# Kernel tuning notes

Hardware: AMD Instinct MI355X
Metric: run time of the kernel (lower is better)

## Reference

```python
import jax, jax.numpy as jnp
import numpy as np

OUTLINER_RATIO = 0.01
SUB_OUTLINER_BIT = 8
NEG_INF = -1e9


def setup_inputs() -> dict:
    key = jax.random.key(0)
    T, H, D = 4096, 8, 64
    qkv = jax.random.normal(key, (T, 3, H, D), dtype=jnp.float32)
    cu_seqlens = jnp.array([0, 1024, 2048, 3072, 4096], dtype=jnp.int32)
    return {"qkv": qkv, "cu_seqlens": cu_seqlens, "max_seqlen": 1024}


def _varlen_attention(q, k, v, cu_seqlens, causal=False):
    # q,k,v: [T, H, D]; sequences delimited by cu_seqlens (attention never
    # crosses segment boundaries, matching flash_attn_varlen semantics).
    T, H, D = q.shape
    scale = D ** (-0.5)
    pos = jnp.arange(T)
    seg = jnp.searchsorted(cu_seqlens, pos, side="right") - 1  # [T] segment ids
    mask = seg[:, None] == seg[None, :]                          # [T, T]
    if causal:
        mask = mask & (pos[:, None] >= pos[None, :])
    scores = jnp.einsum("thd,shd->hts", q, k) * scale            # [H, T, T]
    scores = jnp.where(mask[None, :, :], scores, NEG_INF)
    probs = jax.nn.softmax(scores, axis=-1)
    out = jnp.einsum("hts,shd->thd", probs, v)                   # [T, H, D]
    return out


def _outlier_quant_compress(x, outliner_ratio=OUTLINER_RATIO, bit=SUB_OUTLINER_BIT):
    # Outlier detection: keep top-ratio |x| entries in full precision;
    # quantize the residual (sub-outliers) to `bit` bits per-tensor.
    a = jnp.abs(x)
    thr = jnp.quantile(a.reshape(-1), 1.0 - outliner_ratio)
    outliers = jnp.where(a > thr, x, 0.0)
    resid = x - outliers
    qmax = 2.0 ** (bit - 1) - 1.0
    scale = jnp.maximum(jnp.max(jnp.abs(resid)), 1e-8) / qmax
    q = jnp.clip(jnp.round(resid / scale), -qmax, qmax)
    x_hat = outliers + q * scale  # decompressed approximation
    return x_hat, thr, scale


def reference(qkv, cu_seqlens, max_seqlen):
    q, k, v = qkv[:, 0], qkv[:, 1], qkv[:, 2]
    out = _varlen_attention(q, k, v, cu_seqlens, causal=False)
    # Compression pipeline (stats + quantize) runs on Q,K,V,O in the original
    # forward; it does not alter the forward output.
    for t in (q, k, v, out):
        _outlier_quant_compress(t)
    return out
```

## Files before the change

kernel.cpp:

```cpp
#include <hip/hip_runtime.h>


#define HEADS 8
#define DH 64
#define TQ 64
#define TK 64
#define PSTR 72
#define NEG_BIG -1e30f
#define L2E 1.44269504088896340736f

using f32x4 = __attribute__((ext_vector_type(4))) float;
using s16x8 = __attribute__((ext_vector_type(8))) short;

__device__ inline unsigned short bf16b(float x) {
    union { float f; unsigned u; } c; c.f = x;
    unsigned r = c.u + 0x7fffu + ((c.u >> 16) & 1u);
    return (unsigned short)(r >> 16);
}

#if __has_builtin(__builtin_amdgcn_cvt_pk_bf16_f32)
__device__ inline unsigned pk2(float a, float b) {
    auto v = __builtin_amdgcn_cvt_pk_bf16_f32(a, b);
    unsigned u; __builtin_memcpy(&u, &v, 4); return u;
}
#else
__device__ inline unsigned pk2(float a, float b) {
    return (unsigned)bf16b(a) | ((unsigned)bf16b(b) << 16);
}
#endif

__global__ __launch_bounds__(256)
void prep_kernel(const float* __restrict__ qkv, unsigned short* __restrict__ Qb,
                 unsigned short* __restrict__ Kb, unsigned short* __restrict__ Vtb,
                 int T) {
    __shared__ unsigned short Lt[64][PSTR];
    const int m = blockIdx.z, h = blockIdx.y, t0 = blockIdx.x * 64;
    const int tid = threadIdx.x, d8 = tid & 7, tr = tid >> 3;

    #pragma unroll
    for (int i = 0; i < 2; ++i) {
        int t = t0 + i * 32 + tr;
        int tc = t < T ? t : T - 1;
        const float* src = qkv + ((size_t)tc * 3 + m) * (HEADS * DH) + h * DH + d8 * 8;
        float4 a = *(const float4*)src;
        float4 b = *(const float4*)(src + 4);
        if (m == 0) {
            a.x *= 0.125f; a.y *= 0.125f; a.z *= 0.125f; a.w *= 0.125f;
            b.x *= 0.125f; b.y *= 0.125f; b.z *= 0.125f; b.w *= 0.125f;
        }
        unsigned p0 = pk2(a.x, a.y), p1 = pk2(a.z, a.w);
        unsigned p2 = pk2(b.x, b.y), p3 = pk2(b.z, b.w);
        if (m == 2) {
            *(uint2*)&Lt[i * 32 + tr][d8 * 8]     = make_uint2(p0, p1);
            *(uint2*)&Lt[i * 32 + tr][d8 * 8 + 4] = make_uint2(p2, p3);
        } else if (t < T) {
            unsigned short* dst = (m == 0)
                ? (Qb + (size_t)t * (HEADS * DH) + h * DH + d8 * 8)
                : (Kb + ((size_t)h * T + t) * DH + d8 * 8);
            *(uint4*)dst = make_uint4(p0, p1, p2, p3);
        }
    }
    if (m == 2) {
        __syncthreads();
        const int d = tid >> 2, tg = tid & 3;
        #pragma unroll
        for (int p = 0; p < 2; ++p) {
            int G = tg + 4 * p;
            int td = t0 + G * 8;
            unsigned u[4];
            #pragma unroll
            for (int jj = 0; jj < 4; ++jj)
                u[jj] = (unsigned)Lt[G * 8 + 2 * jj][d] |
                        ((unsigned)Lt[G * 8 + 2 * jj + 1][d] << 16);
            if (td < T)
                *(uint4*)(Vtb + ((size_t)h * DH + d) * T + td) =
                    make_uint4(u[0], u[1], u[2], u[3]);
        }
    }
}

__global__ __launch_bounds__(256, 4)
void fa_main(const unsigned short* __restrict__ Qb, const unsigned short* __restrict__ Kb,
             const unsigned short* __restrict__ Vtb, const int* __restrict__ cu,
             int n_cu, int T, float* __restrict__ out,
             float* __restrict__ Opart, float* __restrict__ Mp, float* __restrict__ Lp) {
    __shared__ unsigned short Ksh[TK * DH];
    __shared__ unsigned short Vsh[DH * TK];
    __shared__ unsigned short Psh[TQ][PSTR];

    const int tid = threadIdx.x;
    const int h = blockIdx.y, t0 = blockIdx.x * TQ;
    const int split = blockIdx.z, nsplit = gridDim.z;
    const int w = tid >> 6, lane = tid & 63, n15 = lane & 15, quad = lane >> 4;

    int trow = t0 + w * 16 + n15; if (trow > T - 1) trow = T - 1;
    int lo, hi;
    { int s = 0; for (int j = 1; j < n_cu - 1; ++j) if (cu[j] <= trow) s = j;
      lo = cu[s]; hi = cu[s + 1]; }
    int kb_, ke;
    { int s = 0; for (int j = 1; j < n_cu - 1; ++j) if (cu[j] <= t0) s = j;
      kb_ = cu[s];
      int tl = t0 + TQ - 1; if (tl > T - 1) tl = T - 1;
      s = 0; for (int j = 1; j < n_cu - 1; ++j) if (cu[j] <= tl) s = j;
      ke = cu[s + 1]; }

    s16x8 qfrag[2];
    {
        int tc = t0 + w * 16 + n15; if (tc > T - 1) tc = T - 1;
        const unsigned short* qp = Qb + (size_t)tc * (HEADS * DH) + h * DH + quad * 8;
        qfrag[0] = *(const s16x8*)qp;
        qfrag[1] = *(const s16x8*)(qp + 32);
    }

    const unsigned short* kb_h = Kb + (size_t)h * T * DH;
    const unsigned short* vt_h = Vtb + (size_t)h * DH * T;
    int krow_rel[2], vkey_off[2];
    const unsigned short* kbase[2];
    const unsigned short* vbase[2];
    #pragma unroll
    for (int i = 0; i < 2; ++i) {
        int gg = i * 64 + lane;
        int rr = gg >> 3;
        int gc = gg & 7;
        int row = w * 16 + rr;
        int gcol = gc ^ (row & 7);
        krow_rel[i] = row;
        kbase[i] = kb_h + gcol * 8;
        vbase[i] = vt_h + (size_t)row * T;
        vkey_off[i] = gcol * 8;
    }
    int off16[2];
    #pragma unroll
    for (int kh = 0; kh < 2; ++kh)
        off16[kh] = n15 * 128 + (((kh * 4 + quad) ^ (n15 & 7)) * 16);

    f32x4 oacc[4];
    #pragma unroll
    for (int i = 0; i < 4; ++i) oacc[i] = (f32x4){0.f, 0.f, 0.f, 0.f};
    float m_ = NEG_BIG, l_ = 0.f;

    const int c0_start = (kb_ / TK) * TK + split * TK;
    for (int c0 = c0_start; c0 < ke; c0 += nsplit * TK) {
        #pragma unroll
        for (int i = 0; i < 2; ++i) {
            int rk = c0 + krow_rel[i]; if (rk > T - 1) rk = T - 1;
            __builtin_amdgcn_global_load_lds(
                (const __attribute__((address_space(1))) void*)(kbase[i] + ((size_t)rk << 6)),
                (__attribute__((address_space(3))) void*)&Ksh[(w * 128 + i * 64) * 8],
                16, 0, 0);
            int kv = c0 + vkey_off[i]; if (kv > T - 8) kv = T - 8;
            __builtin_amdgcn_global_load_lds(
                (const __attribute__((address_space(1))) void*)(vbase[i] + kv),
                (__attribute__((address_space(3))) void*)&Vsh[(w * 128 + i * 64) * 8],
                16, 0, 0);
        }
        __syncthreads();

        const char* Kc = (const char*)Ksh;
        f32x4 sacc[4];
        #pragma unroll
        for (int nt = 0; nt < 4; ++nt) {
            s16x8 k0 = *(const s16x8*)(Kc + nt * 2048 + off16[0]);
            s16x8 k1 = *(const s16x8*)(Kc + nt * 2048 + off16[1]);
            f32x4 z = (f32x4){0.f, 0.f, 0.f, 0.f};
            z = __builtin_amdgcn_mfma_f32_16x16x32_bf16(k0, qfrag[0], z, 0, 0, 0);
            z = __builtin_amdgcn_mfma_f32_16x16x32_bf16(k1, qfrag[1], z, 0, 0, 0);
            sacc[nt] = z;
        }

        if (!(c0 >= lo && c0 + TK <= hi)) {
            #pragma unroll
            for (int nt = 0; nt < 4; ++nt)
                #pragma unroll
                for (int reg = 0; reg < 4; ++reg) {
                    int key = c0 + nt * 16 + quad * 4 + reg;
                    bool valid = (key >= lo) && (key < hi);
                    sacc[nt][reg] = valid ? sacc[nt][reg] : NEG_BIG;
                }
        }

        float rm = NEG_BIG;
        #pragma unroll
        for (int nt = 0; nt < 4; ++nt)
            #pragma unroll
            for (int reg = 0; reg < 4; ++reg) rm = fmaxf(rm, sacc[nt][reg]);
        rm = fmaxf(rm, __shfl_xor(rm, 16));
        rm = fmaxf(rm, __shfl_xor(rm, 32));
        float mn = fmaxf(m_, rm);
        float alpha = exp2f((m_ - mn) * L2E);
        float mnl = mn * L2E;
        float rs = 0.f;
        #pragma unroll
        for (int nt = 0; nt < 4; ++nt) {
            float p0 = exp2f(fmaf(sacc[nt][0], L2E, -mnl));
            float p1 = exp2f(fmaf(sacc[nt][1], L2E, -mnl));
            float p2 = exp2f(fmaf(sacc[nt][2], L2E, -mnl));
            float p3 = exp2f(fmaf(sacc[nt][3], L2E, -mnl));
            rs += (p0 + p1) + (p2 + p3);
            *(uint2*)&Psh[w * 16 + n15][nt * 16 + quad * 4] =
                make_uint2(pk2(p0, p1), pk2(p2, p3));
        }
        rs += __shfl_xor(rs, 16);
        rs += __shfl_xor(rs, 32);
        l_ = fmaf(l_, alpha, rs);
        m_ = mn;
        #pragma unroll
        for (int reg = 0; reg < 4; ++reg) {
            float ar = __shfl(alpha, quad * 4 + reg);
            oacc[0][reg] *= ar; oacc[1][reg] *= ar;
            oacc[2][reg] *= ar; oacc[3][reg] *= ar;
        }

        s16x8 afr[2];
        afr[0] = *(const s16x8*)&Psh[w * 16 + n15][quad * 8];
        afr[1] = *(const s16x8*)&Psh[w * 16 + n15][32 + quad * 8];
        const char* Vc = (const char*)Vsh;
        #pragma unroll
        for (int nt = 0; nt < 4; ++nt) {
            s16x8 v0 = *(const s16x8*)(Vc + nt * 2048 + off16[0]);
            s16x8 v1 = *(const s16x8*)(Vc + nt * 2048 + off16[1]);
            oacc[nt] = __builtin_amdgcn_mfma_f32_16x16x32_bf16(afr[0], v0, oacc[nt], 0, 0, 0);
            oacc[nt] = __builtin_amdgcn_mfma_f32_16x16x32_bf16(afr[1], v1, oacc[nt], 0, 0, 0);
        }
        __syncthreads();
    }

    if (nsplit == 1) {
        #pragma unroll
        for (int reg = 0; reg < 4; ++reg) {
            float lr = __shfl(l_, quad * 4 + reg);
            float inv = 1.f / fmaxf(lr, 1e-30f);
            int t = t0 + w * 16 + quad * 4 + reg;
            if (t < T) {
                #pragma unroll
                for (int nt = 0; nt < 4; ++nt)
                    out[((size_t)t * HEADS + h) * DH + nt * 16 + n15] = oacc[nt][reg] * inv;
            }
        }
    } else {
        #pragma unroll
        for (int reg = 0; reg < 4; ++reg) {
            int t = t0 + w * 16 + quad * 4 + reg;
            if (t < T) {
                size_t base = (((size_t)split * T + t) * HEADS + h) * DH;
                #pragma unroll
                for (int nt = 0; nt < 4; ++nt)
                    Opart[base + nt * 16 + n15] = oacc[nt][reg];
            }
        }
        int tq = t0 + w * 16 + n15;
        if (quad == 0 && tq < T) {
            size_t mi = ((size_t)split * T + tq) * HEADS + h;
            Mp[mi] = m_; Lp[mi] = l_;
        }
    }
}

__global__ __launch_bounds__(256)
void fa_combine_kernel(const float* __restrict__ Opart, const float* __restrict__ Mp,
                       const float* __restrict__ Lp, float* __restrict__ out, int T) {
    int i4 = blockIdx.x * blockDim.x + threadIdx.x;
    int total = T * HEADS * (DH / 4);
    if (i4 >= total) return;
    int th = i4 / (DH / 4);
    int d4 = i4 - th * (DH / 4);
    size_t stride = (size_t)T * HEADS * DH;
    int mlstride = T * HEADS;
    float m0 = Mp[th], m1 = Mp[mlstride + th];
    float l0 = Lp[th], l1 = Lp[mlstride + th];
    float M = fmaxf(m0, m1);
    float w0 = exp2f((m0 - M) * L2E);
    float w1 = exp2f((m1 - M) * L2E);
    float L = fmaxf(fmaf(l0, w0, l1 * w1), 1e-30f);
    float inv = 1.f / L;
    size_t off = (size_t)th * DH + 4 * d4;
    float4 a = *(const float4*)&Opart[off];
    float4 b = *(const float4*)&Opart[stride + off];
    float4 o;
    o.x = fmaf(a.x, w0, b.x * w1) * inv;
    o.y = fmaf(a.y, w0, b.y * w1) * inv;
    o.z = fmaf(a.z, w0, b.z * w1) * inv;
    o.w = fmaf(a.w, w0, b.w * w1) * inv;
    *(float4*)&out[off] = o;
}

extern "C" void kernel_launch(void* const* d_in, const int* in_sizes, int n_in,
                              void* d_out, int out_size, void* d_ws, size_t ws_size,
                              hipStream_t stream) {
    const float* qkv = (const float*)d_in[0];
    const int* cu    = (const int*)d_in[1];
    const int n_cu   = in_sizes[1];
    const int T      = in_sizes[0] / (3 * HEADS * DH);
    float* out       = (float*)d_out;

    const int NSPLIT = 2;
    size_t elems = (size_t)T * HEADS * DH;

    float* Opart = (float*)d_ws;
    float* Mpp   = Opart + (size_t)NSPLIT * elems;
    float* Lpp   = Mpp + (size_t)NSPLIT * T * HEADS;
    unsigned short* Qb  = (unsigned short*)(Lpp + (size_t)NSPLIT * T * HEADS);
    unsigned short* Kb  = Qb + elems;
    unsigned short* Vtb = Kb + elems;

    int tiles = (T + TQ - 1) / TQ;
    dim3 pgrid(tiles, HEADS, 3);
    prep_kernel<<<pgrid, 256, 0, stream>>>(qkv, Qb, Kb, Vtb, T);

    dim3 grid(tiles, HEADS, NSPLIT);
    fa_main<<<grid, 256, 0, stream>>>(Qb, Kb, Vtb, cu, n_cu, T, out, Opart, Mpp, Lpp);

    int total4 = T * HEADS * (DH / 4);
    fa_combine_kernel<<<(total4 + 255) / 256, 256, 0, stream>>>(Opart, Mpp, Lpp, out, T);
}
```

Before: 105.9 us.

## Double query tile per block to reuse K/V loads and raise KV split count to four

Each warp now processes two 16-row query subtiles (TQ 128), so every K/V tile staged in shared memory feeds twice as many MFMAs. To keep enough blocks in flight, the KV dimension is split four ways instead of two, and the combine kernel is generalized to merge NSPLIT partial results. This trades more registers per thread and larger partial-output traffic (4x Opart) for less K/V load work per query; the prep kernel keeps its 64-row tiling.

```diff
diff --git a/kernel.cpp b/kernel.cpp
--- a/kernel.cpp
+++ b/kernel.cpp
@@ -3,9 +3,10 @@
 
 #define HEADS 8
 #define DH 64
-#define TQ 64
+#define TQ 128
 #define TK 64
 #define PSTR 72
+#define NSPLIT 4
 #define NEG_BIG -1e30f
 #define L2E 1.44269504088896340736f
 
@@ -93,10 +94,14 @@
     const int split = blockIdx.z, nsplit = gridDim.z;
     const int w = tid >> 6, lane = tid & 63, n15 = lane & 15, quad = lane >> 4;
 
-    int trow = t0 + w * 16 + n15; if (trow > T - 1) trow = T - 1;
-    int lo, hi;
-    { int s = 0; for (int j = 1; j < n_cu - 1; ++j) if (cu[j] <= trow) s = j;
-      lo = cu[s]; hi = cu[s + 1]; }
+    int lo[2], hi[2];
+    #pragma unroll
+    for (int mt = 0; mt < 2; ++mt) {
+        int trow = t0 + w * 32 + mt * 16 + n15; if (trow > T - 1) trow = T - 1;
+        int s = 0;
+        for (int j = 1; j < n_cu - 1; ++j) if (cu[j] <= trow) s = j;
+        lo[mt] = cu[s]; hi[mt] = cu[s + 1];
+    }
     int kb_, ke;
     { int s = 0; for (int j = 1; j < n_cu - 1; ++j) if (cu[j] <= t0) s = j;
       kb_ = cu[s];
@@ -104,12 +109,13 @@
       s = 0; for (int j = 1; j < n_cu - 1; ++j) if (cu[j] <= tl) s = j;
       ke = cu[s + 1]; }
 
-    s16x8 qfrag[2];
-    {
-        int tc = t0 + w * 16 + n15; if (tc > T - 1) tc = T - 1;
+    s16x8 qfrag[2][2];
+    #pragma unroll
+    for (int mt = 0; mt < 2; ++mt) {
+        int tc = t0 + w * 32 + mt * 16 + n15; if (tc > T - 1) tc = T - 1;
         const unsigned short* qp = Qb + (size_t)tc * (HEADS * DH) + h * DH + quad * 8;
-        qfrag[0] = *(const s16x8*)qp;
-        qfrag[1] = *(const s16x8*)(qp + 32);
+        qfrag[mt][0] = *(const s16x8*)qp;
+        qfrag[mt][1] = *(const s16x8*)(qp + 32);
     }
 
     const unsigned short* kb_h = Kb + (size_t)h * T * DH;
@@ -134,10 +140,12 @@
     for (int kh = 0; kh < 2; ++kh)
         off16[kh] = n15 * 128 + (((kh * 4 + quad) ^ (n15 & 7)) * 16);
 
-    f32x4 oacc[4];
-    #pragma unroll
-    for (int i = 0; i < 4; ++i) oacc[i] = (f32x4){0.f, 0.f, 0.f, 0.f};
-    float m_ = NEG_BIG, l_ = 0.f;
+    f32x4 oacc[2][4];
+    #pragma unroll
+    for (int mt = 0; mt < 2; ++mt)
+        #pragma unroll
+        for (int i = 0; i < 4; ++i) oacc[mt][i] = (f32x4){0.f, 0.f, 0.f, 0.f};
+    float m_[2] = {NEG_BIG, NEG_BIG}, l_[2] = {0.f, 0.f};
 
     const int c0_start = (kb_ / TK) * TK + split * TK;
     for (int c0 = c0_start; c0 < ke; c0 += nsplit * TK) {
@@ -157,101 +165,116 @@
         __syncthreads();
 
         const char* Kc = (const char*)Ksh;
-        f32x4 sacc[4];
+        f32x4 sacc[2][4];
         #pragma unroll
         for (int nt = 0; nt < 4; ++nt) {
             s16x8 k0 = *(const s16x8*)(Kc + nt * 2048 + off16[0]);
             s16x8 k1 = *(const s16x8*)(Kc + nt * 2048 + off16[1]);
-            f32x4 z = (f32x4){0.f, 0.f, 0.f, 0.f};
-            z = __builtin_amdgcn_mfma_f32_16x16x32_bf16(k0, qfrag[0], z, 0, 0, 0);
-            z = __builtin_amdgcn_mfma_f32_16x16x32_bf16(k1, qfrag[1], z, 0, 0, 0);
-            sacc[nt] = z;
-        }
-
-        if (!(c0 >= lo && c0 + TK <= hi)) {
+            #pragma unroll
+            for (int mt = 0; mt < 2; ++mt) {
+                f32x4 z = (f32x4){0.f, 0.f, 0.f, 0.f};
+                z = __builtin_amdgcn_mfma_f32_16x16x32_bf16(k0, qfrag[mt][0], z, 0, 0, 0);
+                z = __builtin_amdgcn_mfma_f32_16x16x32_bf16(k1, qfrag[mt][1], z, 0, 0, 0);
+                sacc[mt][nt] = z;
+            }
+        }
+
+        #pragma unroll
+        for (int mt = 0; mt < 2; ++mt) {
+            if (!(c0 >= lo[mt] && c0 + TK <= hi[mt])) {
+                #pragma unroll
+                for (int nt = 0; nt < 4; ++nt)
+                    #pragma unroll
+                    for (int reg = 0; reg < 4; ++reg) {
+                        int key = c0 + nt * 16 + quad * 4 + reg;
+                        bool valid = (key >= lo[mt]) && (key < hi[mt]);
+                        sacc[mt][nt][reg] = valid ? sacc[mt][nt][reg] : NEG_BIG;
+                    }
+            }
+            float rm = NEG_BIG;
             #pragma unroll
             for (int nt = 0; nt < 4; ++nt)
                 #pragma unroll
-                for (int reg = 0; reg < 4; ++reg) {
-                    int key = c0 + nt * 16 + quad * 4 + reg;
-                    bool valid = (key >= lo) && (key < hi);
-                    sacc[nt][reg] = valid ? sacc[nt][reg] : NEG_BIG;
-                }
-        }
-
-        float rm = NEG_BIG;
-        #pragma unroll
-        for (int nt = 0; nt < 4; ++nt)
-            #pragma unroll
-            for (int reg = 0; reg < 4; ++reg) rm = fmaxf(rm, sacc[nt][reg]);
-        rm = fmaxf(rm, __shfl_xor(rm, 16));
-        rm = fmaxf(rm, __shfl_xor(rm, 32));
-        float mn = fmaxf(m_, rm);
-        float alpha = exp2f((m_ - mn) * L2E);
-        float mnl = mn * L2E;
-        float rs = 0.f;
-        #pragma unroll
-        for (int nt = 0; nt < 4; ++nt) {
-            float p0 = exp2f(fmaf(sacc[nt][0], L2E, -mnl));
-            float p1 = exp2f(fmaf(sacc[nt][1], L2E, -mnl));
-            float p2 = exp2f(fmaf(sacc[nt][2], L2E, -mnl));
-            float p3 = exp2f(fmaf(sacc[nt][3], L2E, -mnl));
-            rs += (p0 + p1) + (p2 + p3);
-            *(uint2*)&Psh[w * 16 + n15][nt * 16 + quad * 4] =
-                make_uint2(pk2(p0, p1), pk2(p2, p3));
-        }
-        rs += __shfl_xor(rs, 16);
-        rs += __shfl_xor(rs, 32);
-        l_ = fmaf(l_, alpha, rs);
-        m_ = mn;
-        #pragma unroll
-        for (int reg = 0; reg < 4; ++reg) {
-            float ar = __shfl(alpha, quad * 4 + reg);
-            oacc[0][reg] *= ar; oacc[1][reg] *= ar;
-            oacc[2][reg] *= ar; oacc[3][reg] *= ar;
-        }
-
-        s16x8 afr[2];
-        afr[0] = *(const s16x8*)&Psh[w * 16 + n15][quad * 8];
-        afr[1] = *(const s16x8*)&Psh[w * 16 + n15][32 + quad * 8];
+                for (int reg = 0; reg < 4; ++reg) rm = fmaxf(rm, sacc[mt][nt][reg]);
+            rm = fmaxf(rm, __shfl_xor(rm, 16));
+            rm = fmaxf(rm, __shfl_xor(rm, 32));
+            float mn = fmaxf(m_[mt], rm);
+            float alpha = exp2f((m_[mt] - mn) * L2E);
+            float mnl = mn * L2E;
+            float rs = 0.f;
+            int prow = w * 32 + mt * 16 + n15;
+            #pragma unroll
+            for (int nt = 0; nt < 4; ++nt) {
+                float p0 = exp2f(fmaf(sacc[mt][nt][0], L2E, -mnl));
+                float p1 = exp2f(fmaf(sacc[mt][nt][1], L2E, -mnl));
+                float p2 = exp2f(fmaf(sacc[mt][nt][2], L2E, -mnl));
+                float p3 = exp2f(fmaf(sacc[mt][nt][3], L2E, -mnl));
+                rs += (p0 + p1) + (p2 + p3);
+                *(uint2*)&Psh[prow][nt * 16 + quad * 4] =
+                    make_uint2(pk2(p0, p1), pk2(p2, p3));
+            }
+            rs += __shfl_xor(rs, 16);
+            rs += __shfl_xor(rs, 32);
+            l_[mt] = fmaf(l_[mt], alpha, rs);
+            m_[mt] = mn;
+            #pragma unroll
+            for (int reg = 0; reg < 4; ++reg) {
+                float ar = __shfl(alpha, quad * 4 + reg);
+                oacc[mt][0][reg] *= ar; oacc[mt][1][reg] *= ar;
+                oacc[mt][2][reg] *= ar; oacc[mt][3][reg] *= ar;
+            }
+        }
+
+        s16x8 afr[2][2];
+        #pragma unroll
+        for (int mt = 0; mt < 2; ++mt) {
+            afr[mt][0] = *(const s16x8*)&Psh[w * 32 + mt * 16 + n15][quad * 8];
+            afr[mt][1] = *(const s16x8*)&Psh[w * 32 + mt * 16 + n15][32 + quad * 8];
+        }
         const char* Vc = (const char*)Vsh;
         #pragma unroll
         for (int nt = 0; nt < 4; ++nt) {
             s16x8 v0 = *(const s16x8*)(Vc + nt * 2048 + off16[0]);
             s16x8 v1 = *(const s16x8*)(Vc + nt * 2048 + off16[1]);
-            oacc[nt] = __builtin_amdgcn_mfma_f32_16x16x32_bf16(afr[0], v0, oacc[nt], 0, 0, 0);
-            oacc[nt] = __builtin_amdgcn_mfma_f32_16x16x32_bf16(afr[1], v1, oacc[nt], 0, 0, 0);
+            #pragma unroll
+            for (int mt = 0; mt < 2; ++mt) {
+                oacc[mt][nt] = __builtin_amdgcn_mfma_f32_16x16x32_bf16(afr[mt][0], v0, oacc[mt][nt], 0, 0, 0);
+                oacc[mt][nt] = __builtin_amdgcn_mfma_f32_16x16x32_bf16(afr[mt][1], v1, oacc[mt][nt], 0, 0, 0);
+            }
         }
         __syncthreads();
     }
 
-    if (nsplit == 1) {
-        #pragma unroll
-        for (int reg = 0; reg < 4; ++reg) {
-            float lr = __shfl(l_, quad * 4 + reg);
-            float inv = 1.f / fmaxf(lr, 1e-30f);
-            int t = t0 + w * 16 + quad * 4 + reg;
-            if (t < T) {
-                #pragma unroll
-                for (int nt = 0; nt < 4; ++nt)
-                    out[((size_t)t * HEADS + h) * DH + nt * 16 + n15] = oacc[nt][reg] * inv;
-            }
-        }
-    } else {
-        #pragma unroll
-        for (int reg = 0; reg < 4; ++reg) {
-            int t = t0 + w * 16 + quad * 4 + reg;
-            if (t < T) {
-                size_t base = (((size_t)split * T + t) * HEADS + h) * DH;
-                #pragma unroll
-                for (int nt = 0; nt < 4; ++nt)
-                    Opart[base + nt * 16 + n15] = oacc[nt][reg];
-            }
-        }
-        int tq = t0 + w * 16 + n15;
-        if (quad == 0 && tq < T) {
-            size_t mi = ((size_t)split * T + tq) * HEADS + h;
-            Mp[mi] = m_; Lp[mi] = l_;
+    #pragma unroll
+    for (int mt = 0; mt < 2; ++mt) {
+        if (nsplit == 1) {
+            #pragma unroll
+            for (int reg = 0; reg < 4; ++reg) {
+                float lr = __shfl(l_[mt], quad * 4 + reg);
+                float inv = 1.f / fmaxf(lr, 1e-30f);
+                int t = t0 + w * 32 + mt * 16 + quad * 4 + reg;
+                if (t < T) {
+                    #pragma unroll
+                    for (int nt = 0; nt < 4; ++nt)
+                        out[((size_t)t * HEADS + h) * DH + nt * 16 + n15] = oacc[mt][nt][reg] * inv;
+                }
+            }
+        } else {
+            #pragma unroll
+            for (int reg = 0; reg < 4; ++reg) {
+                int t = t0 + w * 32 + mt * 16 + quad * 4 + reg;
+                if (t < T) {
+                    size_t base = (((size_t)split * T + t) * HEADS + h) * DH;
+                    #pragma unroll
+                    for (int nt = 0; nt < 4; ++nt)
+                        Opart[base + nt * 16 + n15] = oacc[mt][nt][reg];
+                }
+            }
+            int tq = t0 + w * 32 + mt * 16 + n15;
+            if (quad == 0 && tq < T) {
+                size_t mi = ((size_t)split * T + tq) * HEADS + h;
+                Mp[mi] = m_[mt]; Lp[mi] = l_[mt];
+            }
         }
     }
 }
@@ -266,21 +289,31 @@
     int d4 = i4 - th * (DH / 4);
     size_t stride = (size_t)T * HEADS * DH;
     int mlstride = T * HEADS;
-    float m0 = Mp[th], m1 = Mp[mlstride + th];
-    float l0 = Lp[th], l1 = Lp[mlstride + th];
-    float M = fmaxf(m0, m1);
-    float w0 = exp2f((m0 - M) * L2E);
-    float w1 = exp2f((m1 - M) * L2E);
-    float L = fmaxf(fmaf(l0, w0, l1 * w1), 1e-30f);
-    float inv = 1.f / L;
+    float m[NSPLIT], l[NSPLIT];
+    float M = NEG_BIG;
+    #pragma unroll
+    for (int s = 0; s < NSPLIT; ++s) {
+        m[s] = Mp[(size_t)s * mlstride + th];
+        l[s] = Lp[(size_t)s * mlstride + th];
+        M = fmaxf(M, m[s]);
+    }
+    float L = 0.f, wgt[NSPLIT];
+    #pragma unroll
+    for (int s = 0; s < NSPLIT; ++s) {
+        wgt[s] = exp2f((m[s] - M) * L2E);
+        L = fmaf(l[s], wgt[s], L);
+    }
+    float inv = 1.f / fmaxf(L, 1e-30f);
     size_t off = (size_t)th * DH + 4 * d4;
-    float4 a = *(const float4*)&Opart[off];
-    float4 b = *(const float4*)&Opart[stride + off];
-    float4 o;
-    o.x = fmaf(a.x, w0, b.x * w1) * inv;
-    o.y = fmaf(a.y, w0, b.y * w1) * inv;
-    o.z = fmaf(a.z, w0, b.z * w1) * inv;
-    o.w = fmaf(a.w, w0, b.w * w1) * inv;
+    float4 o = make_float4(0.f, 0.f, 0.f, 0.f);
+    #pragma unroll
+    for (int s = 0; s < NSPLIT; ++s) {
+        float4 a = *(const float4*)&Opart[(size_t)s * stride + off];
+        float ws = wgt[s];
+        o.x = fmaf(a.x, ws, o.x); o.y = fmaf(a.y, ws, o.y);
+        o.z = fmaf(a.z, ws, o.z); o.w = fmaf(a.w, ws, o.w);
+    }
+    o.x *= inv; o.y *= inv; o.z *= inv; o.w *= inv;
     *(float4*)&out[off] = o;
 }
 
@@ -293,7 +326,6 @@
     const int T      = in_sizes[0] / (3 * HEADS * DH);
     float* out       = (float*)d_out;
 
-    const int NSPLIT = 2;
     size_t elems = (size_t)T * HEADS * DH;
 
     float* Opart = (float*)d_ws;
@@ -303,10 +335,11 @@
     unsigned short* Kb  = Qb + elems;
     unsigned short* Vtb = Kb + elems;
 
+    int ptiles = (T + 63) / 64;
+    dim3 pgrid(ptiles, HEADS, 3);
+    prep_kernel<<<pgrid, 256, 0, stream>>>(qkv, Qb, Kb, Vtb, T);
+
     int tiles = (T + TQ - 1) / TQ;
-    dim3 pgrid(tiles, HEADS, 3);
-    prep_kernel<<<pgrid, 256, 0, stream>>>(qkv, Qb, Kb, Vtb, T);
-
     dim3 grid(tiles, HEADS, NSPLIT);
     fa_main<<<grid, 256, 0, stream>>>(Qb, Kb, Vtb, cu, n_cu, T, out, Opart, Mpp, Lpp);
 
```

Result: slower. 111.8 us (+5.6%).

## Double-buffer K/V tiles in LDS and fuse Q conversion into attention kernel

Applied to the files above, without the earlier changes.

The attention loop now double-buffers the K and V shared-memory tiles, issuing the async global-to-LDS loads for the next chunk before computing on the current one. This lets it drop the trailing barrier so memory latency overlaps with the MFMA work. Q is read straight from the fp32 input and converted to scaled bf16 inside the attention kernel, so the prep kernel no longer writes and re-reads a Q buffer. The doubled LDS use lowers the occupancy hint from 4 to 3 blocks per CU, and the combine kernel is generalised over NSPLIT.

```diff
diff --git a/kernel.cpp b/kernel.cpp
--- a/kernel.cpp
+++ b/kernel.cpp
@@ -6,6 +6,7 @@
 #define TQ 64
 #define TK 64
 #define PSTR 72
+#define NSPLIT 2
 #define NEG_BIG -1e30f
 #define L2E 1.44269504088896340736f
 
@@ -30,11 +31,11 @@
 #endif
 
 __global__ __launch_bounds__(256)
-void prep_kernel(const float* __restrict__ qkv, unsigned short* __restrict__ Qb,
-                 unsigned short* __restrict__ Kb, unsigned short* __restrict__ Vtb,
-                 int T) {
+void prep_kernel(const float* __restrict__ qkv, unsigned short* __restrict__ Kb,
+                 unsigned short* __restrict__ Vtb, int T) {
     __shared__ unsigned short Lt[64][PSTR];
-    const int m = blockIdx.z, h = blockIdx.y, t0 = blockIdx.x * 64;
+    const int m = blockIdx.z + 1;
+    const int h = blockIdx.y, t0 = blockIdx.x * 64;
     const int tid = threadIdx.x, d8 = tid & 7, tr = tid >> 3;
 
     #pragma unroll
@@ -44,20 +45,13 @@
         const float* src = qkv + ((size_t)tc * 3 + m) * (HEADS * DH) + h * DH + d8 * 8;
         float4 a = *(const float4*)src;
         float4 b = *(const float4*)(src + 4);
-        if (m == 0) {
-            a.x *= 0.125f; a.y *= 0.125f; a.z *= 0.125f; a.w *= 0.125f;
-            b.x *= 0.125f; b.y *= 0.125f; b.z *= 0.125f; b.w *= 0.125f;
-        }
         unsigned p0 = pk2(a.x, a.y), p1 = pk2(a.z, a.w);
         unsigned p2 = pk2(b.x, b.y), p3 = pk2(b.z, b.w);
         if (m == 2) {
             *(uint2*)&Lt[i * 32 + tr][d8 * 8]     = make_uint2(p0, p1);
             *(uint2*)&Lt[i * 32 + tr][d8 * 8 + 4] = make_uint2(p2, p3);
         } else if (t < T) {
-            unsigned short* dst = (m == 0)
-                ? (Qb + (size_t)t * (HEADS * DH) + h * DH + d8 * 8)
-                : (Kb + ((size_t)h * T + t) * DH + d8 * 8);
-            *(uint4*)dst = make_uint4(p0, p1, p2, p3);
+            *(uint4*)(Kb + ((size_t)h * T + t) * DH + d8 * 8) = make_uint4(p0, p1, p2, p3);
         }
     }
     if (m == 2) {
@@ -79,13 +73,13 @@
     }
 }
 
-__global__ __launch_bounds__(256, 4)
-void fa_main(const unsigned short* __restrict__ Qb, const unsigned short* __restrict__ Kb,
+__global__ __launch_bounds__(256, 3)
+void fa_main(const float* __restrict__ qkv, const unsigned short* __restrict__ Kb,
              const unsigned short* __restrict__ Vtb, const int* __restrict__ cu,
              int n_cu, int T, float* __restrict__ out,
              float* __restrict__ Opart, float* __restrict__ Mp, float* __restrict__ Lp) {
-    __shared__ unsigned short Ksh[TK * DH];
-    __shared__ unsigned short Vsh[DH * TK];
+    __shared__ unsigned short Ksh[2][TK * DH];
+    __shared__ unsigned short Vsh[2][TK * DH];
     __shared__ unsigned short Psh[TQ][PSTR];
 
     const int tid = threadIdx.x;
@@ -107,14 +101,23 @@
     s16x8 qfrag[2];
     {
         int tc = t0 + w * 16 + n15; if (tc > T - 1) tc = T - 1;
-        const unsigned short* qp = Qb + (size_t)tc * (HEADS * DH) + h * DH + quad * 8;
-        qfrag[0] = *(const s16x8*)qp;
-        qfrag[1] = *(const s16x8*)(qp + 32);
+        const float* qp = qkv + (size_t)tc * 3 * (HEADS * DH) + h * DH + quad * 8;
+        #pragma unroll
+        for (int kh = 0; kh < 2; ++kh) {
+            float4 a = *(const float4*)(qp + kh * 32);
+            float4 b = *(const float4*)(qp + kh * 32 + 4);
+            unsigned u0 = pk2(a.x * 0.125f, a.y * 0.125f);
+            unsigned u1 = pk2(a.z * 0.125f, a.w * 0.125f);
+            unsigned u2 = pk2(b.x * 0.125f, b.y * 0.125f);
+            unsigned u3 = pk2(b.z * 0.125f, b.w * 0.125f);
+            uint4 uu = make_uint4(u0, u1, u2, u3);
+            __builtin_memcpy(&qfrag[kh], &uu, 16);
+        }
     }
 
     const unsigned short* kb_h = Kb + (size_t)h * T * DH;
     const unsigned short* vt_h = Vtb + (size_t)h * DH * T;
-    int krow_rel[2], vkey_off[2];
+    int krow_rel[2], vkey_off[2], ldst[2];
     const unsigned short* kbase[2];
     const unsigned short* vbase[2];
     #pragma unroll
@@ -128,6 +131,7 @@
         kbase[i] = kb_h + gcol * 8;
         vbase[i] = vt_h + (size_t)row * T;
         vkey_off[i] = gcol * 8;
+        ldst[i] = (w * 128 + i * 64) * 8;
     }
     int off16[2];
     #pragma unroll
@@ -139,24 +143,41 @@
     for (int i = 0; i < 4; ++i) oacc[i] = (f32x4){0.f, 0.f, 0.f, 0.f};
     float m_ = NEG_BIG, l_ = 0.f;
 
+    const int step = nsplit * TK;
     const int c0_start = (kb_ / TK) * TK + split * TK;
-    for (int c0 = c0_start; c0 < ke; c0 += nsplit * TK) {
-        #pragma unroll
-        for (int i = 0; i < 2; ++i) {
-            int rk = c0 + krow_rel[i]; if (rk > T - 1) rk = T - 1;
-            __builtin_amdgcn_global_load_lds(
-                (const __attribute__((address_space(1))) void*)(kbase[i] + ((size_t)rk << 6)),
-                (__attribute__((address_space(3))) void*)&Ksh[(w * 128 + i * 64) * 8],
-                16, 0, 0);
-            int kv = c0 + vkey_off[i]; if (kv > T - 8) kv = T - 8;
-            __builtin_amdgcn_global_load_lds(
-                (const __attribute__((address_space(1))) void*)(vbase[i] + kv),
-                (__attribute__((address_space(3))) void*)&Vsh[(w * 128 + i * 64) * 8],
-                16, 0, 0);
-        }
+
+    #pragma unroll
+    for (int i = 0; i < 2; ++i) {
+        int rk = c0_start + krow_rel[i]; if (rk > T - 1) rk = T - 1;
+        __builtin_amdgcn_global_load_lds(
+            (const __attribute__((address_space(1))) void*)(kbase[i] + ((size_t)rk << 6)),
+            (__attribute__((address_space(3))) void*)&Ksh[0][ldst[i]], 16, 0, 0);
+        int kv = c0_start + vkey_off[i]; if (kv > T - 8) kv = T - 8;
+        __builtin_amdgcn_global_load_lds(
+            (const __attribute__((address_space(1))) void*)(vbase[i] + kv),
+            (__attribute__((address_space(3))) void*)&Vsh[0][ldst[i]], 16, 0, 0);
+    }
+
+    int ib = 0;
+    for (int c0 = c0_start; c0 < ke; c0 += step, ib ^= 1) {
         __syncthreads();
 
-        const char* Kc = (const char*)Ksh;
+        int cn = c0 + step;
+        if (cn < ke) {
+            #pragma unroll
+            for (int i = 0; i < 2; ++i) {
+                int rk = cn + krow_rel[i]; if (rk > T - 1) rk = T - 1;
+                __builtin_amdgcn_global_load_lds(
+                    (const __attribute__((address_space(1))) void*)(kbase[i] + ((size_t)rk << 6)),
+                    (__attribute__((address_space(3))) void*)&Ksh[ib ^ 1][ldst[i]], 16, 0, 0);
+                int kv = cn + vkey_off[i]; if (kv > T - 8) kv = T - 8;
+                __builtin_amdgcn_global_load_lds(
+                    (const __attribute__((address_space(1))) void*)(vbase[i] + kv),
+                    (__attribute__((address_space(3))) void*)&Vsh[ib ^ 1][ldst[i]], 16, 0, 0);
+            }
+        }
+
+        const char* Kc = (const char*)Ksh[ib];
         f32x4 sacc[4];
         #pragma unroll
         for (int nt = 0; nt < 4; ++nt) {
@@ -214,7 +235,7 @@
         s16x8 afr[2];
         afr[0] = *(const s16x8*)&Psh[w * 16 + n15][quad * 8];
         afr[1] = *(const s16x8*)&Psh[w * 16 + n15][32 + quad * 8];
-        const char* Vc = (const char*)Vsh;
+        const char* Vc = (const char*)Vsh[ib];
         #pragma unroll
         for (int nt = 0; nt < 4; ++nt) {
             s16x8 v0 = *(const s16x8*)(Vc + nt * 2048 + off16[0]);
@@ -222,7 +243,6 @@
             oacc[nt] = __builtin_amdgcn_mfma_f32_16x16x32_bf16(afr[0], v0, oacc[nt], 0, 0, 0);
             oacc[nt] = __builtin_amdgcn_mfma_f32_16x16x32_bf16(afr[1], v1, oacc[nt], 0, 0, 0);
         }
-        __syncthreads();
     }
 
     if (nsplit == 1) {
@@ -266,21 +286,31 @@
     int d4 = i4 - th * (DH / 4);
     size_t stride = (size_t)T * HEADS * DH;
     int mlstride = T * HEADS;
-    float m0 = Mp[th], m1 = Mp[mlstride + th];
-    float l0 = Lp[th], l1 = Lp[mlstride + th];
-    float M = fmaxf(m0, m1);
-    float w0 = exp2f((m0 - M) * L2E);
-    float w1 = exp2f((m1 - M) * L2E);
-    float L = fmaxf(fmaf(l0, w0, l1 * w1), 1e-30f);
-    float inv = 1.f / L;
+    float m[NSPLIT], l[NSPLIT];
+    float M = NEG_BIG;
+    #pragma unroll
+    for (int s = 0; s < NSPLIT; ++s) {
+        m[s] = Mp[(size_t)s * mlstride + th];
+        l[s] = Lp[(size_t)s * mlstride + th];
+        M = fmaxf(M, m[s]);
+    }
+    float L = 0.f, wgt[NSPLIT];
+    #pragma unroll
+    for (int s = 0; s < NSPLIT; ++s) {
+        wgt[s] = exp2f((m[s] - M) * L2E);
+        L = fmaf(l[s], wgt[s], L);
+    }
+    float inv = 1.f / fmaxf(L, 1e-30f);
     size_t off = (size_t)th * DH + 4 * d4;
-    float4 a = *(const float4*)&Opart[off];
-    float4 b = *(const float4*)&Opart[stride + off];
-    float4 o;
-    o.x = fmaf(a.x, w0, b.x * w1) * inv;
-    o.y = fmaf(a.y, w0, b.y * w1) * inv;
-    o.z = fmaf(a.z, w0, b.z * w1) * inv;
-    o.w = fmaf(a.w, w0, b.w * w1) * inv;
+    float4 o = make_float4(0.f, 0.f, 0.f, 0.f);
+    #pragma unroll
+    for (int s = 0; s < NSPLIT; ++s) {
+        float4 a = *(const float4*)&Opart[(size_t)s * stride + off];
+        float ws = wgt[s];
+        o.x = fmaf(a.x, ws, o.x); o.y = fmaf(a.y, ws, o.y);
+        o.z = fmaf(a.z, ws, o.z); o.w = fmaf(a.w, ws, o.w);
+    }
+    o.x *= inv; o.y *= inv; o.z *= inv; o.w *= inv;
     *(float4*)&out[off] = o;
 }
 
@@ -293,22 +323,21 @@
     const int T      = in_sizes[0] / (3 * HEADS * DH);
     float* out       = (float*)d_out;
 
-    const int NSPLIT = 2;
     size_t elems = (size_t)T * HEADS * DH;
 
     float* Opart = (float*)d_ws;
     float* Mpp   = Opart + (size_t)NSPLIT * elems;
     float* Lpp   = Mpp + (size_t)NSPLIT * T * HEADS;
-    unsigned short* Qb  = (unsigned short*)(Lpp + (size_t)NSPLIT * T * HEADS);
-    unsigned short* Kb  = Qb + elems;
+    unsigned short* Kb  = (unsigned short*)(Lpp + (size_t)NSPLIT * T * HEADS);
     unsigned short* Vtb = Kb + elems;
 
+    int ptiles = (T + 63) / 64;
+    dim3 pgrid(ptiles, HEADS, 2);
+    prep_kernel<<<pgrid, 256, 0, stream>>>(qkv, Kb, Vtb, T);
+
     int tiles = (T + TQ - 1) / TQ;
-    dim3 pgrid(tiles, HEADS, 3);
-    prep_kernel<<<pgrid, 256, 0, stream>>>(qkv, Qb, Kb, Vtb, T);
-
     dim3 grid(tiles, HEADS, NSPLIT);
-    fa_main<<<grid, 256, 0, stream>>>(Qb, Kb, Vtb, cu, n_cu, T, out, Opart, Mpp, Lpp);
+    fa_main<<<grid, 256, 0, stream>>>(qkv, Kb, Vtb, cu, n_cu, T, out, Opart, Mpp, Lpp);
 
     int total4 = T * HEADS * (DH / 4);
     fa_combine_kernel<<<(total4 + 255) / 256, 256, 0, stream>>>(Opart, Mpp, Lpp, out, T);
```

Result: slower. 109.4 us (+3.3%).
